# Optimization experiments

Hardware: AMD Instinct MI355X
Metric: run time of the kernel (lower is better)

Reference implementation:

```python
import jax, jax.numpy as jnp
import numpy as np

WIN_SIZE = 11
WIN_SIGMA = 1.5
DATA_RANGE = 1.0
ALPHA = 1.0
K1, K2 = 0.01, 0.03
WEIGHTS = jnp.array([0.0448, 0.2856, 0.3001, 0.2363, 0.1333], dtype=jnp.float32)


def _gauss_win(size, sigma):
    coords = jnp.arange(size, dtype=jnp.float32) - size // 2
    g = jnp.exp(-(coords ** 2) / (2.0 * sigma * sigma))
    return g / g.sum()


def _gfilter(x, win):
    # separable depthwise Gaussian blur, VALID padding (matches pytorch_msssim)
    C = x.shape[1]
    ws = win.shape[0]
    dn = ('NCHW', 'OIHW', 'NCHW')
    kh = jnp.broadcast_to(win.reshape(1, 1, 1, ws), (C, 1, 1, ws))
    kv = jnp.broadcast_to(win.reshape(1, 1, ws, 1), (C, 1, ws, 1))
    x = jax.lax.conv_general_dilated(x, kh, (1, 1), 'VALID', dimension_numbers=dn, feature_group_count=C)
    x = jax.lax.conv_general_dilated(x, kv, (1, 1), 'VALID', dimension_numbers=dn, feature_group_count=C)
    return x


def _ssim(X, Y, win):
    C1 = (K1 * DATA_RANGE) ** 2
    C2 = (K2 * DATA_RANGE) ** 2
    mu1 = _gfilter(X, win)
    mu2 = _gfilter(Y, win)
    mu1_sq, mu2_sq, mu1_mu2 = mu1 * mu1, mu2 * mu2, mu1 * mu2
    sigma1_sq = _gfilter(X * X, win) - mu1_sq
    sigma2_sq = _gfilter(Y * Y, win) - mu2_sq
    sigma12 = _gfilter(X * Y, win) - mu1_mu2
    cs_map = (2.0 * sigma12 + C2) / (sigma1_sq + sigma2_sq + C2)
    ssim_map = ((2.0 * mu1_mu2 + C1) / (mu1_sq + mu2_sq + C1)) * cs_map
    return ssim_map.mean(axis=(2, 3)), cs_map.mean(axis=(2, 3))  # (B,C) each


def _avgpool2(x):
    # 2x2 avg pool, stride 2 (all dims even for 512 -> 32 pyramid, so no padding)
    B, C, H, W = x.shape
    return x.reshape(B, C, H // 2, 2, W // 2, 2).mean(axis=(3, 5))


def _ms_ssim(X, Y):
    win = _gauss_win(WIN_SIZE, WIN_SIGMA)
    levels = WEIGHTS.shape[0]
    mcs = []
    ssim_pc = None
    for i in range(levels):
        ssim_pc, cs = _ssim(X, Y, win)
        if i < levels - 1:
            mcs.append(jax.nn.relu(cs))
            X = _avgpool2(X)
            Y = _avgpool2(Y)
    m = jnp.stack(mcs + [jax.nn.relu(ssim_pc)])  # (levels, B, C)
    val = jnp.prod(m ** WEIGHTS.reshape(-1, 1, 1), axis=0)  # (B, C)
    return val.mean()  # size_average=True


def setup_inputs() -> dict:
    key = jax.random.key(0)
    k1, k2 = jax.random.split(key)
    logits = jax.random.normal(k1, (4, 29, 512, 512), dtype=jnp.float32)
    targets = jnp.round(jax.random.uniform(k2, (4, 29, 512, 512), dtype=jnp.float32))
    return {"logits": logits, "targets": targets}


def reference(logits, targets):
    probs = jax.nn.sigmoid(logits)
    ms_ssim_val = _ms_ssim(probs, targets)
    loss = ALPHA * (1.0 - ms_ssim_val)
    return jnp.mean(loss)  # reduction='mean' on a scalar
```

## Files before the change

kernel.cpp:

```cpp
#include <hip/hip_runtime.h>
#include <math.h>

#define NIMG 116
#define TW 118
#define TH 16

static constexpr float W[11] = {
    0.00102838f, 0.00759876f, 0.03600078f, 0.10936075f, 0.21300554f,
    0.26601172f, 0.21300554f, 0.10936075f, 0.03600078f, 0.00759876f,
    0.00102838f};

typedef float f2 __attribute__((ext_vector_type(2)));

__device__ __forceinline__ f2 pkfma(f2 a, f2 b, f2 c) {
#if __has_builtin(__builtin_elementwise_fma)
    return __builtin_elementwise_fma(a, b, c);
#else
    f2 r; r.x = fmaf(a.x, b.x, c.x); r.y = fmaf(a.y, b.y, c.y); return r;
#endif
}

__device__ __forceinline__ float frcp(float x) {
    return __builtin_amdgcn_rcpf(x);
}

__device__ __forceinline__ float fsig(float x) {
    float e = __builtin_amdgcn_exp2f(x * -1.4426950408889634f);
    return frcp(1.0f + e);
}

template <int N, int M, bool SIG, bool POOL, bool SKIPYY, bool NARROW>
__device__ __forceinline__ void ssim_tile(
    const float* __restrict__ X, const float* __restrict__ Y,
    float* __restrict__ accSsim, float* __restrict__ accCs,
    float* __restrict__ poolX, float* __restrict__ poolY,
    int img, int bx, int by, float* smem) {
    const int tid = threadIdx.x;
    const int ox0 = NARROW ? 0 : bx * TW;
    const int oy0 = by * TH;
    const long base = (long)img * N * N;

    const int c  = tid & 127;
    const int s  = tid >> 7;
    const int ci = ox0 + c;
    constexpr int half = N >> 1;
    const int powned = NARROW ? N : min(TW, N - ox0);

    const float* __restrict__ Xb = X + base;
    const float* __restrict__ Yb = Y + base;

    const bool interior = (oy0 + 25 < N) && (ox0 + 127 < N);

    f2 xy[18];
    if (interior) {
        const float* __restrict__ xp = Xb + (long)(oy0 + 8 * s) * N + ci;
        const float* __restrict__ yp = Yb + (long)(oy0 + 8 * s) * N + ci;
#pragma unroll
        for (int i = 0; i < 18; i++) {
            xy[i].x = xp[(long)i * N];
            xy[i].y = yp[(long)i * N];
        }
    } else {
        const int cic = min(ci, N - 1);
#pragma unroll
        for (int i = 0; i < 18; i++) {
            int rc = min(oy0 + 8 * s + i, N - 1);
            xy[i].x = Xb[(long)rc * N + cic];
            xy[i].y = Yb[(long)rc * N + cic];
        }
    }
    __builtin_amdgcn_sched_barrier(0);

    if (SIG) {
#pragma unroll
        for (int i = 0; i < 18; i++) xy[i].x = fsig(xy[i].x);
    }

    f2 WP[11];
#pragma unroll
    for (int t = 0; t < 11; t++) WP[t] = (f2){W[t], W[t]};
    asm volatile("" ::
        "v"(WP[0]), "v"(WP[1]), "v"(WP[2]), "v"(WP[3]), "v"(WP[4]),
        "v"(WP[5]), "v"(WP[6]), "v"(WP[7]), "v"(WP[8]), "v"(WP[9]),
        "v"(WP[10]));

    f2 a01[8], a23[8];
    float ayy[SKIPYY ? 1 : 8];
#pragma unroll
    for (int o = 0; o < 8; o++) {
        a01[o] = (f2){0.f, 0.f};
        a23[o] = (f2){0.f, 0.f};
        if constexpr (!SKIPYY) ayy[o] = 0.f;
    }

#pragma unroll
    for (int i = 0; i < 18; i++) {
        f2 v01 = xy[i];
        f2 xb = (f2){v01.x, v01.x};
        f2 v23 = xb * v01;
        float yy;
        if constexpr (!SKIPYY) yy = v01.y * v01.y;
#pragma unroll
        for (int o = 0; o < 8; o++) {
            int t = i - o;
            if (t >= 0 && t < 11) {
                a01[o] = pkfma(WP[t], v01, a01[o]);
                a23[o] = pkfma(WP[t], v23, a23[o]);
                if constexpr (!SKIPYY) ayy[o] = fmaf(W[t], yy, ayy[o]);
            }
        }
    }

    if (POOL) {
        float cx[4], cy[4];
#pragma unroll
        for (int p = 0; p < 4; p++) {
            cx[p] = xy[2 * p].x + xy[2 * p + 1].x;
            cy[p] = xy[2 * p].y + xy[2 * p + 1].y;
        }
#pragma unroll
        for (int p = 0; p < 4; p++) {
            float rx = __shfl_down(cx[p], 1, 64);
            float ry = __shfl_down(cy[p], 1, 64);
            if (!(c & 1) && c < powned) {
                int orow = (oy0 + 8 * s + 2 * p) >> 1;
                int ocol = ci >> 1;
                long pb = (long)img * half * half + (long)orow * half + ocol;
                poolX[pb] = 0.25f * (cx[p] + rx);
                poolY[pb] = 0.25f * (cy[p] + ry);
            }
        }
    }

#pragma unroll
    for (int o = 0; o < 8; o++) {
        int rr = 8 * s + o;
        int phys = c ^ (((c >> 3) + rr) & 7);
        float4 v;
        v.x = a01[o].x; v.y = a01[o].y; v.z = a23[o].x; v.w = a23[o].y;
        *(float4*)&smem[rr * 512 + phys * 4] = v;
        if constexpr (!SKIPYY) {
            int ch = c >> 2;
            int pc = ch ^ (((ch >> 3) + rr) & 7);
            smem[8192 + rr * 128 + pc * 4 + (c & 3)] = ayy[o];
        }
    }
    __syncthreads();

    const float C1 = 1e-4f, C2 = 9e-4f;
    float scs = 0.f, sss = 0.f;
    {
        const int r = tid >> 4;
        const int k = tid & 15;
        if (k < 15) {
            f2 a01h[8], a23h[8];
#pragma unroll
            for (int j = 0; j < 8; j++) {
                a01h[j] = (f2){0.f, 0.f};
                a23h[j] = (f2){0.f, 0.f};
            }
#pragma unroll
            for (int m = 0; m < 18; m++) {
                int col = 8 * k + m;
                int g = (k + (m >> 3) + r) & 7;
                int phys = (col ^ g) & 127;
                const float4 v4 = *(const float4*)&smem[r * 512 + phys * 4];
                f2 v01 = (f2){v4.x, v4.y};
                f2 v23 = (f2){v4.z, v4.w};
#pragma unroll
                for (int j = 0; j < 8; j++) {
                    int t = m - j;
                    if (t >= 0 && t < 11) {
                        a01h[j] = pkfma(WP[t], v01, a01h[j]);
                        a23h[j] = pkfma(WP[t], v23, a23h[j]);
                    }
                }
            }
            float oyy[8];
            if constexpr (!SKIPYY) {
                float rgs[20];
#pragma unroll
                for (int j5 = 0; j5 < 5; j5++) {
                    int ch = 2 * k + j5;
                    int pc = (ch ^ (((ch >> 3) + r) & 7)) & 31;
                    const float4 v4 = *(const float4*)&smem[8192 + r * 128 + pc * 4];
                    rgs[4 * j5 + 0] = v4.x; rgs[4 * j5 + 1] = v4.y;
                    rgs[4 * j5 + 2] = v4.z; rgs[4 * j5 + 3] = v4.w;
                }
#pragma unroll
                for (int j = 0; j < 8; j++) {
                    float a = 0.f;
#pragma unroll
                    for (int t = 0; t < 11; t++) a = fmaf(W[t], rgs[j + t], a);
                    oyy[j] = a;
                }
            }
            const int gy = oy0 + r;
            const bool rowok = gy < M;
#pragma unroll
            for (int j = 0; j < 8; j++) {
                int lc = 8 * k + j;
                int gx = ox0 + lc;
                if (lc < TW && gx < M && rowok) {
                    float mu1 = a01h[j].x, mu2 = a01h[j].y;
                    float exx = a23h[j].x, exy = a23h[j].y;
                    float m11 = mu1 * mu1, m22 = mu2 * mu2, m12 = mu1 * mu2;
                    float s1 = exx - m11;
                    float s2 = SKIPYY ? (mu2 - m22) : (oyy[j] - m22);
                    float s12 = exy - m12;
                    float cs = (2.f * s12 + C2) * frcp(s1 + s2 + C2);
                    float ssim = (2.f * m12 + C1) * frcp(m11 + m22 + C1) * cs;
                    scs += cs; sss += ssim;
                }
            }
        }
    }

    for (int off = 32; off > 0; off >>= 1) {
        scs += __shfl_down(scs, off, 64);
        sss += __shfl_down(sss, off, 64);
    }
    __syncthreads();
    int lane = tid & 63, wv = tid >> 6;
    if (lane == 0) { smem[wv] = scs; smem[4 + wv] = sss; }
    __syncthreads();
    if (tid == 0) {
        atomicAdd(&accCs[img],   smem[0] + smem[1] + smem[2] + smem[3]);
        atomicAdd(&accSsim[img], smem[4] + smem[5] + smem[6] + smem[7]);
    }
}

template <int N, int M, bool SIG, bool POOL, bool SKIPYY, bool NARROW>
__global__ __launch_bounds__(256, 4)
void ssim_kernel(const float* __restrict__ X, const float* __restrict__ Y,
                 float* __restrict__ accSsim, float* __restrict__ accCs,
                 float* __restrict__ poolX, float* __restrict__ poolY) {
    __shared__ float smem[10240];
    ssim_tile<N, M, SIG, POOL, SKIPYY, NARROW>(X, Y, accSsim, accCs, poolX, poolY,
                                               blockIdx.z, blockIdx.x, blockIdx.y, smem);
}

__global__ __launch_bounds__(128)
void finalize_kernel(const float* __restrict__ acc, float* __restrict__ out) {
    const float wts[5] = {0.0448f, 0.2856f, 0.3001f, 0.2363f, 0.1333f};
    const int Ms[5] = {502, 246, 118, 54, 22};
    int t = threadIdx.x;
    float v = 0.f;
    if (t < NIMG) {
        float prod = 1.f;
#pragma unroll
        for (int l = 0; l < 5; l++) {
            float inv = 1.0f / ((float)Ms[l] * (float)Ms[l]);
            float m = (l < 4) ? acc[l * 2 * NIMG + NIMG + t] * inv
                              : acc[l * 2 * NIMG + t] * inv;
            m = fmaxf(m, 0.f);
            prod *= powf(m, wts[l]);
        }
        v = prod;
    }
    for (int off = 32; off > 0; off >>= 1) v += __shfl_down(v, off, 64);
    __shared__ float red[2];
    if ((t & 63) == 0) red[t >> 6] = v;
    __syncthreads();
    if (t == 0) out[0] = 1.0f - (red[0] + red[1]) / (float)NIMG;
}

extern "C" void kernel_launch(void* const* d_in, const int* in_sizes, int n_in,
                              void* d_out, int out_size, void* d_ws, size_t ws_size,
                              hipStream_t stream) {
    const float* logits = (const float*)d_in[0];
    const float* targets = (const float*)d_in[1];
    float* out = (float*)d_out;
    float* ws = (float*)d_ws;

    float* acc = ws;
    size_t off = 1280;
    float* X1 = ws + off; off += (size_t)NIMG * 256 * 256;
    float* Y1 = ws + off; off += (size_t)NIMG * 256 * 256;
    float* X2 = ws + off; off += (size_t)NIMG * 128 * 128;
    float* Y2 = ws + off; off += (size_t)NIMG * 128 * 128;
    float* X3 = ws + off; off += (size_t)NIMG * 64 * 64;
    float* Y3 = ws + off; off += (size_t)NIMG * 64 * 64;
    float* X4 = ws + off; off += (size_t)NIMG * 32 * 32;
    float* Y4 = ws + off; off += (size_t)NIMG * 32 * 32;

    hipMemsetAsync(acc, 0, 1160 * sizeof(float), stream);

    {
        dim3 grid((512 + TW - 1) / TW, 512 / TH, NIMG);
        ssim_kernel<512, 502, true, true, true, false><<<grid, 256, 0, stream>>>(
            logits, targets, acc, acc + NIMG, X1, Y1);
    }
    {
        dim3 grid((256 + TW - 1) / TW, 256 / TH, NIMG);
        ssim_kernel<256, 246, false, true, false, false><<<grid, 256, 0, stream>>>(
            X1, Y1, acc + 2 * NIMG, acc + 3 * NIMG, X2, Y2);
    }
    {
        dim3 grid(1, 128 / TH, NIMG);
        ssim_kernel<128, 118, false, true, false, true><<<grid, 256, 0, stream>>>(
            X2, Y2, acc + 4 * NIMG, acc + 5 * NIMG, X3, Y3);
    }
    {
        dim3 grid(1, 64 / TH, NIMG);
        ssim_kernel<64, 54, false, true, false, true><<<grid, 256, 0, stream>>>(
            X3, Y3, acc + 6 * NIMG, acc + 7 * NIMG, X4, Y4);
    }
    {
        dim3 grid(1, 32 / TH, NIMG);
        ssim_kernel<32, 22, false, false, false, true><<<grid, 256, 0, stream>>>(
            X4, Y4, acc + 8 * NIMG, acc + 9 * NIMG, nullptr, nullptr);
    }

    finalize_kernel<<<1, 128, 0, stream>>>(acc, out);
}
```

Measured before the change: 416.0 us.

## Process two row tiles per block and overlap next tile load with horizontal pass

For the two largest pyramid levels, each block now handles two vertically adjacent tiles. The global loads for the second tile are issued before the horizontal filter pass of the first tile, so load latency can be hidden behind compute. This halves the number of blocks and their atomics and amortizes setup. The cost is higher register pressure from holding two 18-element tiles, which may cause spills or lower occupancy, plus an extra barrier. The asm volatile pinning the weights in registers was also dropped.

Result: slower. 444.0 us (+6.7%).

```diff
diff --git a/kernel.cpp b/kernel.cpp
--- a/kernel.cpp
+++ b/kernel.cpp
@@ -29,127 +29,117 @@
     return frcp(1.0f + e);
 }
 
-template <int N, int M, bool SIG, bool POOL, bool SKIPYY, bool NARROW>
-__device__ __forceinline__ void ssim_tile(
-    const float* __restrict__ X, const float* __restrict__ Y,
-    float* __restrict__ accSsim, float* __restrict__ accCs,
-    float* __restrict__ poolX, float* __restrict__ poolY,
-    int img, int bx, int by, float* smem) {
+template <int N, int M, bool SIG, bool POOL, bool SKIPYY, bool NARROW, bool PIPE2>
+__global__ __launch_bounds__(256, 4)
+void ssim_kernel(const float* __restrict__ X, const float* __restrict__ Y,
+                 float* __restrict__ accSsim, float* __restrict__ accCs,
+                 float* __restrict__ poolX, float* __restrict__ poolY) {
+    __shared__ float smem[10240];
     const int tid = threadIdx.x;
-    const int ox0 = NARROW ? 0 : bx * TW;
-    const int oy0 = by * TH;
-    const long base = (long)img * N * N;
-
+    const int img = blockIdx.z;
+    const int ox0 = NARROW ? 0 : blockIdx.x * TW;
     const int c  = tid & 127;
     const int s  = tid >> 7;
     const int ci = ox0 + c;
     constexpr int half = N >> 1;
     const int powned = NARROW ? N : min(TW, N - ox0);
-
+    const long base = (long)img * N * N;
     const float* __restrict__ Xb = X + base;
     const float* __restrict__ Yb = Y + base;
 
-    const bool interior = (oy0 + 25 < N) && (ox0 + 127 < N);
-
-    f2 xy[18];
-    if (interior) {
-        const float* __restrict__ xp = Xb + (long)(oy0 + 8 * s) * N + ci;
-        const float* __restrict__ yp = Yb + (long)(oy0 + 8 * s) * N + ci;
+    f2 WP[11];
+#pragma unroll
+    for (int t = 0; t < 11; t++) WP[t] = (f2){W[t], W[t]};
+
+    auto load_tile = [&](int oy0, f2* xy) {
+        const bool interior = (oy0 + 25 < N) && (ox0 + 127 < N);
+        if (interior) {
+            const float* __restrict__ xp = Xb + (long)(oy0 + 8 * s) * N + ci;
+            const float* __restrict__ yp = Yb + (long)(oy0 + 8 * s) * N + ci;
+#pragma unroll
+            for (int i = 0; i < 18; i++) {
+                xy[i].x = xp[(long)i * N];
+                xy[i].y = yp[(long)i * N];
+            }
+        } else {
+            const int cic = min(ci, N - 1);
+#pragma unroll
+            for (int i = 0; i < 18; i++) {
+                int rc = min(oy0 + 8 * s + i, N - 1);
+                xy[i].x = Xb[(long)rc * N + cic];
+                xy[i].y = Yb[(long)rc * N + cic];
+            }
+        }
+        __builtin_amdgcn_sched_barrier(0);
+    };
+
+    auto vert_store = [&](int oy0, f2* xy) {
+        if constexpr (SIG) {
+#pragma unroll
+            for (int i = 0; i < 18; i++) xy[i].x = fsig(xy[i].x);
+        }
+        f2 a01[8], a23[8];
+        float ayy[SKIPYY ? 1 : 8];
+#pragma unroll
+        for (int o = 0; o < 8; o++) {
+            a01[o] = (f2){0.f, 0.f};
+            a23[o] = (f2){0.f, 0.f};
+            if constexpr (!SKIPYY) ayy[o] = 0.f;
+        }
 #pragma unroll
         for (int i = 0; i < 18; i++) {
-            xy[i].x = xp[(long)i * N];
-            xy[i].y = yp[(long)i * N];
-        }
-    } else {
-        const int cic = min(ci, N - 1);
-#pragma unroll
-        for (int i = 0; i < 18; i++) {
-            int rc = min(oy0 + 8 * s + i, N - 1);
-            xy[i].x = Xb[(long)rc * N + cic];
-            xy[i].y = Yb[(long)rc * N + cic];
-        }
-    }
-    __builtin_amdgcn_sched_barrier(0);
-
-    if (SIG) {
-#pragma unroll
-        for (int i = 0; i < 18; i++) xy[i].x = fsig(xy[i].x);
-    }
-
-    f2 WP[11];
-#pragma unroll
-    for (int t = 0; t < 11; t++) WP[t] = (f2){W[t], W[t]};
-    asm volatile("" ::
-        "v"(WP[0]), "v"(WP[1]), "v"(WP[2]), "v"(WP[3]), "v"(WP[4]),
-        "v"(WP[5]), "v"(WP[6]), "v"(WP[7]), "v"(WP[8]), "v"(WP[9]),
-        "v"(WP[10]));
-
-    f2 a01[8], a23[8];
-    float ayy[SKIPYY ? 1 : 8];
-#pragma unroll
-    for (int o = 0; o < 8; o++) {
-        a01[o] = (f2){0.f, 0.f};
-        a23[o] = (f2){0.f, 0.f};
-        if constexpr (!SKIPYY) ayy[o] = 0.f;
-    }
-
-#pragma unroll
-    for (int i = 0; i < 18; i++) {
-        f2 v01 = xy[i];
-        f2 xb = (f2){v01.x, v01.x};
-        f2 v23 = xb * v01;
-        float yy;
-        if constexpr (!SKIPYY) yy = v01.y * v01.y;
+            f2 v01 = xy[i];
+            f2 xb = (f2){v01.x, v01.x};
+            f2 v23 = xb * v01;
+            float yy;
+            if constexpr (!SKIPYY) yy = v01.y * v01.y;
+#pragma unroll
+            for (int o = 0; o < 8; o++) {
+                int t = i - o;
+                if (t >= 0 && t < 11) {
+                    a01[o] = pkfma(WP[t], v01, a01[o]);
+                    a23[o] = pkfma(WP[t], v23, a23[o]);
+                    if constexpr (!SKIPYY) ayy[o] = fmaf(W[t], yy, ayy[o]);
+                }
+            }
+        }
+        if constexpr (POOL) {
+            float cx[4], cy[4];
+#pragma unroll
+            for (int p = 0; p < 4; p++) {
+                cx[p] = xy[2 * p].x + xy[2 * p + 1].x;
+                cy[p] = xy[2 * p].y + xy[2 * p + 1].y;
+            }
+#pragma unroll
+            for (int p = 0; p < 4; p++) {
+                float rx = __shfl_down(cx[p], 1, 64);
+                float ry = __shfl_down(cy[p], 1, 64);
+                if (!(c & 1) && c < powned) {
+                    int orow = (oy0 + 8 * s + 2 * p) >> 1;
+                    int ocol = ci >> 1;
+                    long pb = (long)img * half * half + (long)orow * half + ocol;
+                    poolX[pb] = 0.25f * (cx[p] + rx);
+                    poolY[pb] = 0.25f * (cy[p] + ry);
+                }
+            }
+        }
 #pragma unroll
         for (int o = 0; o < 8; o++) {
-            int t = i - o;
-            if (t >= 0 && t < 11) {
-                a01[o] = pkfma(WP[t], v01, a01[o]);
-                a23[o] = pkfma(WP[t], v23, a23[o]);
-                if constexpr (!SKIPYY) ayy[o] = fmaf(W[t], yy, ayy[o]);
-            }
-        }
-    }
-
-    if (POOL) {
-        float cx[4], cy[4];
-#pragma unroll
-        for (int p = 0; p < 4; p++) {
-            cx[p] = xy[2 * p].x + xy[2 * p + 1].x;
-            cy[p] = xy[2 * p].y + xy[2 * p + 1].y;
-        }
-#pragma unroll
-        for (int p = 0; p < 4; p++) {
-            float rx = __shfl_down(cx[p], 1, 64);
-            float ry = __shfl_down(cy[p], 1, 64);
-            if (!(c & 1) && c < powned) {
-                int orow = (oy0 + 8 * s + 2 * p) >> 1;
-                int ocol = ci >> 1;
-                long pb = (long)img * half * half + (long)orow * half + ocol;
-                poolX[pb] = 0.25f * (cx[p] + rx);
-                poolY[pb] = 0.25f * (cy[p] + ry);
-            }
-        }
-    }
-
-#pragma unroll
-    for (int o = 0; o < 8; o++) {
-        int rr = 8 * s + o;
-        int phys = c ^ (((c >> 3) + rr) & 7);
-        float4 v;
-        v.x = a01[o].x; v.y = a01[o].y; v.z = a23[o].x; v.w = a23[o].y;
-        *(float4*)&smem[rr * 512 + phys * 4] = v;
-        if constexpr (!SKIPYY) {
-            int ch = c >> 2;
-            int pc = ch ^ (((ch >> 3) + rr) & 7);
-            smem[8192 + rr * 128 + pc * 4 + (c & 3)] = ayy[o];
-        }
-    }
-    __syncthreads();
+            int rr = 8 * s + o;
+            int phys = c ^ (((c >> 3) + rr) & 7);
+            float4 v;
+            v.x = a01[o].x; v.y = a01[o].y; v.z = a23[o].x; v.w = a23[o].y;
+            *(float4*)&smem[rr * 512 + phys * 4] = v;
+            if constexpr (!SKIPYY) {
+                int ch = c >> 2;
+                int pc = ch ^ (((ch >> 3) + rr) & 7);
+                smem[8192 + rr * 128 + pc * 4 + (c & 3)] = ayy[o];
+            }
+        }
+    };
 
     const float C1 = 1e-4f, C2 = 9e-4f;
-    float scs = 0.f, sss = 0.f;
-    {
+    auto phase2 = [&](int oy0, float& scs, float& sss) {
         const int r = tid >> 4;
         const int k = tid & 15;
         if (k < 15) {
@@ -214,6 +204,29 @@
                 }
             }
         }
+    };
+
+    float scs = 0.f, sss = 0.f;
+    if constexpr (PIPE2) {
+        const int oyA = (int)(blockIdx.y * 2) * TH;
+        const int oyB = oyA + TH;
+        f2 xyA[18], xyB[18];
+        load_tile(oyA, xyA);
+        vert_store(oyA, xyA);
+        __syncthreads();
+        load_tile(oyB, xyB);
+        phase2(oyA, scs, sss);
+        __syncthreads();
+        vert_store(oyB, xyB);
+        __syncthreads();
+        phase2(oyB, scs, sss);
+    } else {
+        const int oy0 = blockIdx.y * TH;
+        f2 xy[18];
+        load_tile(oy0, xy);
+        vert_store(oy0, xy);
+        __syncthreads();
+        phase2(oy0, scs, sss);
     }
 
     for (int off = 32; off > 0; off >>= 1) {
@@ -228,16 +241,6 @@
         atomicAdd(&accCs[img],   smem[0] + smem[1] + smem[2] + smem[3]);
         atomicAdd(&accSsim[img], smem[4] + smem[5] + smem[6] + smem[7]);
     }
-}
-
-template <int N, int M, bool SIG, bool POOL, bool SKIPYY, bool NARROW>
-__global__ __launch_bounds__(256, 4)
-void ssim_kernel(const float* __restrict__ X, const float* __restrict__ Y,
-                 float* __restrict__ accSsim, float* __restrict__ accCs,
-                 float* __restrict__ poolX, float* __restrict__ poolY) {
-    __shared__ float smem[10240];
-    ssim_tile<N, M, SIG, POOL, SKIPYY, NARROW>(X, Y, accSsim, accCs, poolX, poolY,
-                                               blockIdx.z, blockIdx.x, blockIdx.y, smem);
 }
 
 __global__ __launch_bounds__(128)
@@ -287,28 +290,28 @@
     hipMemsetAsync(acc, 0, 1160 * sizeof(float), stream);
 
     {
-        dim3 grid((512 + TW - 1) / TW, 512 / TH, NIMG);
-        ssim_kernel<512, 502, true, true, true, false><<<grid, 256, 0, stream>>>(
+        dim3 grid((512 + TW - 1) / TW, 512 / TH / 2, NIMG);
+        ssim_kernel<512, 502, true, true, true, false, true><<<grid, 256, 0, stream>>>(
             logits, targets, acc, acc + NIMG, X1, Y1);
     }
     {
-        dim3 grid((256 + TW - 1) / TW, 256 / TH, NIMG);
-        ssim_kernel<256, 246, false, true, false, false><<<grid, 256, 0, stream>>>(
+        dim3 grid((256 + TW - 1) / TW, 256 / TH / 2, NIMG);
+        ssim_kernel<256, 246, false, true, false, false, true><<<grid, 256, 0, stream>>>(
             X1, Y1, acc + 2 * NIMG, acc + 3 * NIMG, X2, Y2);
     }
     {
         dim3 grid(1, 128 / TH, NIMG);
-        ssim_kernel<128, 118, false, true, false, true><<<grid, 256, 0, stream>>>(
+        ssim_kernel<128, 118, false, true, false, true, false><<<grid, 256, 0, stream>>>(
             X2, Y2, acc + 4 * NIMG, acc + 5 * NIMG, X3, Y3);
     }
     {
         dim3 grid(1, 64 / TH, NIMG);
-        ssim_kernel<64, 54, false, true, false, true><<<grid, 256, 0, stream>>>(
+        ssim_kernel<64, 54, false, true, false, true, false><<<grid, 256, 0, stream>>>(
             X3, Y3, acc + 6 * NIMG, acc + 7 * NIMG, X4, Y4);
     }
     {
         dim3 grid(1, 32 / TH, NIMG);
-        ssim_kernel<32, 22, false, false, false, true><<<grid, 256, 0, stream>>>(
+        ssim_kernel<32, 22, false, false, false, true, false><<<grid, 256, 0, stream>>>(
             X4, Y4, acc + 8 * NIMG, acc + 9 * NIMG, nullptr, nullptr);
     }
 
```
